# Optimization experiments

Measured on AMD Instinct MI355X. Metric: run time of the kernel, lower is better.

Reference implementation:

```python
import jax, jax.numpy as jnp
import numpy as np

MARGIN = 0.2
EPS = 1e-6  # F.pairwise_distance default eps (added to the difference)


def _cdist(x):
    # Euclidean pairwise distances, [N, N]
    sq = jnp.sum(x * x, axis=1)
    d2 = sq[:, None] + sq[None, :] - 2.0 * (x @ x.T)
    return jnp.sqrt(jnp.maximum(d2, 0.0))


def setup_inputs() -> dict:
    key = jax.random.key(0)
    k1, k2 = jax.random.split(key)
    features = jax.random.normal(k1, (8192, 128), dtype=jnp.float32)
    labels = jax.random.randint(k2, (8192,), 0, 512)
    return {"features": features, "labels": labels}


def reference(features, labels):
    # Distances are used only for (non-differentiable) index selection.
    dists = jax.lax.stop_gradient(_cdist(features))
    pos_mask = labels[None, :] == labels[:, None]  # includes diagonal (self), as in the torch loop
    neg_mask = ~pos_mask

    # Batch-hard mining, vectorized over all anchor rows:
    # hardest positive = max dist among same-label; hardest negative = min dist among different-label.
    pos_idx = jnp.argmax(jnp.where(pos_mask, dists, -jnp.inf), axis=1)
    neg_idx = jnp.argmin(jnp.where(neg_mask, dists, jnp.inf), axis=1)
    # Anchor is skipped in the original loop only if it has no negatives.
    valid = jnp.any(neg_mask, axis=1)

    anchors = features
    pos = features[pos_idx]
    neg = features[neg_idx]

    # F.pairwise_distance(x1, x2, p=2) == ||x1 - x2 + eps||_2
    pos_d = jnp.linalg.norm(anchors - pos + EPS, axis=1)
    neg_d = jnp.linalg.norm(anchors - neg + EPS, axis=1)
    per_anchor = jax.nn.relu(pos_d - neg_d + MARGIN)

    cnt = jnp.sum(valid)
    loss = jnp.where(
        cnt > 0,
        jnp.sum(jnp.where(valid, per_anchor, 0.0)) / jnp.maximum(cnt, 1).astype(per_anchor.dtype),
        jnp.zeros((), per_anchor.dtype),
    )
    return loss
```

## Files before the change

kernel.cpp:

```cpp
#include <hip/hip_runtime.h>
#include <hip/hip_bf16.h>

#define N 8192
#define DIMS 128
#define NSLICE 16
#define SLICE_COLS (N / NSLICE)
#define SUBTILES (SLICE_COLS / 16)
#define NSTEPS (SUBTILES / 2)
#define ROWS_PER_BLOCK 128
#define STRIPS 2
#define NROWBLK (N / ROWS_PER_BLOCK)
#define NFIN 2048
#define MARGIN_F 0.2f
#define EPS_F 1e-6f
#define INF_F __builtin_huge_valf()

typedef __bf16 bf16x8 __attribute__((ext_vector_type(8)));
typedef float f32x4 __attribute__((ext_vector_type(4)));

#define XB_OFF   0
#define META_OFF 2097152
#define PART_OFF 2162688
#define BSUM_OFF 4259840

#define GLD_LDS(g, l) \
  __builtin_amdgcn_global_load_lds( \
      (const __attribute__((address_space(1))) void*)(g), \
      (__attribute__((address_space(3))) void*)(l), 16, 0, 0)

__global__ __launch_bounds__(256) void prep_kernel(
    const float* __restrict__ feat, const int* __restrict__ lab,
    unsigned short* __restrict__ Xb, float2* __restrict__ meta) {
  int row = blockIdx.x * 4 + (threadIdx.x >> 6);
  int lane = threadIdx.x & 63;
  float2 x = *reinterpret_cast<const float2*>(feat + (size_t)row * DIMS + lane * 2);
  __hip_bfloat16 hx = __float2bfloat16(x.x);
  __hip_bfloat16 hy = __float2bfloat16(x.y);
  unsigned short ux, uy;
  __builtin_memcpy(&ux, &hx, 2);
  __builtin_memcpy(&uy, &hy, 2);
  unsigned int packed = (unsigned int)ux | ((unsigned int)uy << 16);
  *reinterpret_cast<unsigned int*>(Xb + (size_t)row * DIMS + lane * 2) = packed;
  float s = x.x * x.x + x.y * x.y;
#pragma unroll
  for (int m = 32; m >= 1; m >>= 1) s += __shfl_xor(s, m, 64);
  if (lane == 0) meta[row] = make_float2(s, __int_as_float(lab[row]));
}

__global__ __launch_bounds__(256, 4) void mine_kernel(
    const unsigned short* __restrict__ Xb, const float2* __restrict__ meta,
    const int* __restrict__ lab, float4* __restrict__ part) {
  __shared__ char smem[2 * 8192 + 4096];

  int rb = blockIdx.x / NSLICE;
  int sl = blockIdx.x % NSLICE;
  int tid = threadIdx.x;
  int wave = tid >> 6;
  int lane = tid & 63;
  int lrow = lane & 15;
  int lk = lane >> 4;
  int rowbase = rb * ROWS_PER_BLOCK + wave * (STRIPS * 16);
  int j0 = sl * SLICE_COLS;

  {
    const char* g = (const char*)meta + (size_t)j0 * 8 + tid * 16;
    char* l = smem + 16384 + wave * 1024;
    GLD_LDS(g, l);
  }
  int colt = tid >> 4;
  int chunk = tid & 15;
  const char* gsrc0 = (const char*)Xb + (size_t)(j0 + colt) * 256 +
                      ((chunk ^ (colt & 7)) * 16);
  {
    GLD_LDS(gsrc0, smem + wave * 1024);
    GLD_LDS(gsrc0 + 16 * 256, smem + 4096 + wave * 1024);
  }

  bf16x8 afrag[STRIPS][4];
#pragma unroll
  for (int s = 0; s < STRIPS; ++s) {
    const unsigned short* rp = Xb + (size_t)(rowbase + s * 16 + lrow) * DIMS;
#pragma unroll
    for (int g = 0; g < 4; ++g)
      afrag[s][g] = *reinterpret_cast<const bf16x8*>(rp + g * 32 + lk * 8);
  }
  int4 labi[STRIPS];
#pragma unroll
  for (int s = 0; s < STRIPS; ++s)
    labi[s] = *reinterpret_cast<const int4*>(lab + rowbase + s * 16 + lk * 4);

  float bpv[STRIPS][4], bnv[STRIPS][4];
  int bpi[STRIPS][4], bni[STRIPS][4];
#pragma unroll
  for (int s = 0; s < STRIPS; ++s)
#pragma unroll
    for (int e = 0; e < 4; ++e) {
      bpv[s][e] = -INF_F; bnv[s][e] = INF_F; bpi[s][e] = 0; bni[s][e] = 0;
    }

  int boff[4];
#pragma unroll
  for (int g = 0; g < 4; ++g)
    boff[g] = lrow * 256 + (((g * 4 + lk) ^ (lrow & 7)) * 16);

  __syncthreads();

  for (int it = 0; it < NSTEPS; ++it) {
    int cur = it & 1;
    if (it + 1 < NSTEPS) {
      const char* g = gsrc0 + (size_t)(it + 1) * 8192;
      char* l = smem + (cur ^ 1) * 8192 + wave * 1024;
      GLD_LDS(g, l);
      GLD_LDS(g + 16 * 256, l + 4096);
    }

#pragma unroll
    for (int h = 0; h < 2; ++h) {
      int t = it * 2 + h;
      float2 mcur =
          *reinterpret_cast<const float2*>(smem + 16384 + t * 128 + lrow * 8);
      float sqj = mcur.x;
      int labj = __float_as_int(mcur.y);
      int jcur = j0 + t * 16 + lrow;

      const char* bbase = smem + cur * 8192 + h * 4096;
      bf16x8 bb[4];
#pragma unroll
      for (int g = 0; g < 4; ++g)
        bb[g] = *reinterpret_cast<const bf16x8*>(bbase + boff[g]);

#pragma unroll
      for (int s = 0; s < STRIPS; ++s) {
        f32x4 acc = {0.f, 0.f, 0.f, 0.f};
#pragma unroll
        for (int g = 0; g < 4; ++g)
          acc = __builtin_amdgcn_mfma_f32_16x16x32_bf16(afrag[s][g], bb[g], acc,
                                                        0, 0, 0);
        int labs[4] = {labi[s].x, labi[s].y, labi[s].z, labi[s].w};
#pragma unroll
        for (int e = 0; e < 4; ++e) {
          float key = fmaf(-2.0f, acc[e], sqj);
          bool pos = (labj == labs[e]);
          bool gp = pos && (key > bpv[s][e]);
          bool gn = (!pos) && (key < bnv[s][e]);
          bpv[s][e] = gp ? key : bpv[s][e];
          bpi[s][e] = gp ? jcur : bpi[s][e];
          bnv[s][e] = gn ? key : bnv[s][e];
          bni[s][e] = gn ? jcur : bni[s][e];
        }
      }
    }
    __syncthreads();
  }

#pragma unroll
  for (int s = 0; s < STRIPS; ++s) {
#pragma unroll
    for (int e = 0; e < 4; ++e) {
      float pv = bpv[s][e]; int pi = bpi[s][e];
      float nv = bnv[s][e]; int ni = bni[s][e];
#pragma unroll
      for (int m = 1; m < 16; m <<= 1) {
        float opv = __shfl_xor(pv, m, 64); int opi = __shfl_xor(pi, m, 64);
        float onv = __shfl_xor(nv, m, 64); int oni = __shfl_xor(ni, m, 64);
        bool tp = (opv > pv) || (opv == pv && opi < pi);
        pv = tp ? opv : pv; pi = tp ? opi : pi;
        bool tn = (onv < nv) || (onv == nv && oni < ni);
        nv = tn ? onv : nv; ni = tn ? oni : ni;
      }
      if (lrow == 0) {
        int row = rowbase + s * 16 + lk * 4 + e;
        part[(size_t)sl * N + row] =
            make_float4(pv, __int_as_float(pi), nv, __int_as_float(ni));
      }
    }
  }
}

__global__ __launch_bounds__(256) void finalize_kernel(
    const float* __restrict__ feat, const float4* __restrict__ part,
    float2* __restrict__ bsum) {
  int wave = threadIdx.x >> 6, lane = threadIdx.x & 63;
  int i = blockIdx.x * 4 + wave;

  float pv = -INF_F, nv = INF_F;
  int pi = 0, ni = 0;
  if (lane < NSLICE) {
    float4 p = part[(size_t)lane * N + i];
    pv = p.x; pi = __float_as_int(p.y);
    nv = p.z; ni = __float_as_int(p.w);
  }
#pragma unroll
  for (int m = 1; m < 16; m <<= 1) {
    float opv = __shfl_xor(pv, m, 64); int opi = __shfl_xor(pi, m, 64);
    float onv = __shfl_xor(nv, m, 64); int oni = __shfl_xor(ni, m, 64);
    bool tp = (opv > pv) || (opv == pv && opi < pi);
    pv = tp ? opv : pv; pi = tp ? opi : pi;
    bool tn = (onv < nv) || (onv == nv && oni < ni);
    nv = tn ? onv : nv; ni = tn ? oni : ni;
  }
  pi = __shfl(pi, 0, 64);
  ni = __shfl(ni, 0, 64);
  float nvb = __shfl(nv, 0, 64);
  bool valid = (nvb < INF_F);

  float2 av = *reinterpret_cast<const float2*>(feat + (size_t)i * DIMS + lane * 2);
  float2 pw = *reinterpret_cast<const float2*>(feat + (size_t)pi * DIMS + lane * 2);
  float2 nw = *reinterpret_cast<const float2*>(feat + (size_t)ni * DIMS + lane * 2);
  float d0 = av.x - pw.x + EPS_F, d1 = av.y - pw.y + EPS_F;
  float sp = fmaf(d0, d0, d1 * d1);
  float e0 = av.x - nw.x + EPS_F, e1 = av.y - nw.y + EPS_F;
  float sn = fmaf(e0, e0, e1 * e1);
#pragma unroll
  for (int m = 32; m >= 1; m >>= 1) {
    sp += __shfl_xor(sp, m, 64);
    sn += __shfl_xor(sn, m, 64);
  }

  __shared__ float s_s[4], s_c[4];
  if (lane == 0) {
    float per = sqrtf(sp) - sqrtf(sn) + MARGIN_F;
    per = per > 0.f ? per : 0.f;
    per = valid ? per : 0.f;
    s_s[wave] = per;
    s_c[wave] = valid ? 1.f : 0.f;
  }
  __syncthreads();
  if (threadIdx.x == 0) {
    float ts = (s_s[0] + s_s[1]) + (s_s[2] + s_s[3]);
    float tc = (s_c[0] + s_c[1]) + (s_c[2] + s_c[3]);
    bsum[blockIdx.x] = make_float2(ts, tc);
  }
}

__global__ __launch_bounds__(256) void final_reduce_kernel(
    const float2* __restrict__ bsum, float* __restrict__ out) {
  int t = threadIdx.x;
  float s = 0.f, c = 0.f;
#pragma unroll
  for (int k = 0; k < NFIN / 256; ++k) {
    float2 v = bsum[t + k * 256];
    s += v.x; c += v.y;
  }
#pragma unroll
  for (int m = 32; m >= 1; m >>= 1) {
    s += __shfl_xor(s, m, 64);
    c += __shfl_xor(c, m, 64);
  }
  __shared__ float s_s[4], s_c[4];
  int wave = t >> 6, lane = t & 63;
  if (lane == 0) { s_s[wave] = s; s_c[wave] = c; }
  __syncthreads();
  if (t == 0) {
    float ts = (s_s[0] + s_s[1]) + (s_s[2] + s_s[3]);
    float tc = (s_c[0] + s_c[1]) + (s_c[2] + s_c[3]);
    out[0] = (tc > 0.f) ? (ts / tc) : 0.f;
  }
}

extern "C" void kernel_launch(void* const* d_in, const int* in_sizes, int n_in,
                              void* d_out, int out_size, void* d_ws, size_t ws_size,
                              hipStream_t stream) {
  const float* feat = (const float*)d_in[0];
  const int* lab = (const int*)d_in[1];
  char* ws = (char*)d_ws;
  unsigned short* Xb = (unsigned short*)(ws + XB_OFF);
  float2* meta = (float2*)(ws + META_OFF);
  float4* part = (float4*)(ws + PART_OFF);
  float2* bsum = (float2*)(ws + BSUM_OFF);
  float* out = (float*)d_out;

  prep_kernel<<<N / 4, 256, 0, stream>>>(feat, lab, Xb, meta);
  mine_kernel<<<NROWBLK * NSLICE, 256, 0, stream>>>(Xb, meta, lab, part);
  finalize_kernel<<<N / 4, 256, 0, stream>>>(feat, part, bsum);
  final_reduce_kernel<<<1, 256, 0, stream>>>(bsum, out);
}
```

Baseline: 49.46 us.

## Pack distance key and column index into one uint for integer max/min mining

Adds a positive bias to the squared norms so that every distance key stays positive. Each key's float bits are truncated and the 13-bit column index is ORed into the low bits, so the argmax/argmin tracking becomes a single unsigned max/min per element. This removes the separate compare/select of value and index, halves the partial-result storage, and simplifies both shuffle reductions. The tiling also changes to 256 rows per block with 4 strips and 32 column slices, which raises register reuse but lowers occupancy. Truncating the low mantissa bits can change ties and near-ties in hard-example selection, and it relies on the bias keeping keys positive for these inputs.

```diff
diff --git a/kernel.cpp b/kernel.cpp
--- a/kernel.cpp
+++ b/kernel.cpp
@@ -3,16 +3,17 @@
 
 #define N 8192
 #define DIMS 128
-#define NSLICE 16
+#define NSLICE 32
 #define SLICE_COLS (N / NSLICE)
 #define SUBTILES (SLICE_COLS / 16)
 #define NSTEPS (SUBTILES / 2)
-#define ROWS_PER_BLOCK 128
-#define STRIPS 2
+#define ROWS_PER_BLOCK 256
+#define STRIPS 4
 #define NROWBLK (N / ROWS_PER_BLOCK)
 #define NFIN 2048
 #define MARGIN_F 0.2f
 #define EPS_F 1e-6f
+#define BIAS_F 512.0f
 #define INF_F __builtin_huge_valf()
 
 typedef __bf16 bf16x8 __attribute__((ext_vector_type(8)));
@@ -44,13 +45,13 @@
   float s = x.x * x.x + x.y * x.y;
 #pragma unroll
   for (int m = 32; m >= 1; m >>= 1) s += __shfl_xor(s, m, 64);
-  if (lane == 0) meta[row] = make_float2(s, __int_as_float(lab[row]));
-}
-
-__global__ __launch_bounds__(256, 4) void mine_kernel(
+  if (lane == 0) meta[row] = make_float2(s + BIAS_F, __int_as_float(lab[row]));
+}
+
+__global__ __launch_bounds__(256, 3) void mine_kernel(
     const unsigned short* __restrict__ Xb, const float2* __restrict__ meta,
-    const int* __restrict__ lab, float4* __restrict__ part) {
-  __shared__ char smem[2 * 8192 + 4096];
+    const int* __restrict__ lab, uint2* __restrict__ part) {
+  __shared__ char smem[2 * 8192 + 2048];
 
   int rb = blockIdx.x / NSLICE;
   int sl = blockIdx.x % NSLICE;
@@ -62,7 +63,7 @@
   int rowbase = rb * ROWS_PER_BLOCK + wave * (STRIPS * 16);
   int j0 = sl * SLICE_COLS;
 
-  {
+  if (wave < 2) {
     const char* g = (const char*)meta + (size_t)j0 * 8 + tid * 16;
     char* l = smem + 16384 + wave * 1024;
     GLD_LDS(g, l);
@@ -73,7 +74,7 @@
                       ((chunk ^ (colt & 7)) * 16);
   {
     GLD_LDS(gsrc0, smem + wave * 1024);
-    GLD_LDS(gsrc0 + 16 * 256, smem + 4096 + wave * 1024);
+    GLD_LDS(gsrc0 + 4096, smem + 4096 + wave * 1024);
   }
 
   bf16x8 afrag[STRIPS][4];
@@ -89,14 +90,11 @@
   for (int s = 0; s < STRIPS; ++s)
     labi[s] = *reinterpret_cast<const int4*>(lab + rowbase + s * 16 + lk * 4);
 
-  float bpv[STRIPS][4], bnv[STRIPS][4];
-  int bpi[STRIPS][4], bni[STRIPS][4];
+  unsigned int bpu[STRIPS][4], bnu[STRIPS][4];
 #pragma unroll
   for (int s = 0; s < STRIPS; ++s)
 #pragma unroll
-    for (int e = 0; e < 4; ++e) {
-      bpv[s][e] = -INF_F; bnv[s][e] = INF_F; bpi[s][e] = 0; bni[s][e] = 0;
-    }
+    for (int e = 0; e < 4; ++e) { bpu[s][e] = 0u; bnu[s][e] = 0xFFFFFFFFu; }
 
   int boff[4];
 #pragma unroll
@@ -111,7 +109,7 @@
       const char* g = gsrc0 + (size_t)(it + 1) * 8192;
       char* l = smem + (cur ^ 1) * 8192 + wave * 1024;
       GLD_LDS(g, l);
-      GLD_LDS(g + 16 * 256, l + 4096);
+      GLD_LDS(g + 4096, l + 4096);
     }
 
 #pragma unroll
@@ -119,9 +117,9 @@
       int t = it * 2 + h;
       float2 mcur =
           *reinterpret_cast<const float2*>(smem + 16384 + t * 128 + lrow * 8);
-      float sqj = mcur.x;
+      float sqjB = mcur.x;
       int labj = __float_as_int(mcur.y);
-      int jcur = j0 + t * 16 + lrow;
+      unsigned int ju = (unsigned int)(j0 + t * 16 + lrow);
 
       const char* bbase = smem + cur * 8192 + h * 4096;
       bf16x8 bb[4];
@@ -139,14 +137,13 @@
         int labs[4] = {labi[s].x, labi[s].y, labi[s].z, labi[s].w};
 #pragma unroll
         for (int e = 0; e < 4; ++e) {
-          float key = fmaf(-2.0f, acc[e], sqj);
+          float key = fmaf(-2.0f, acc[e], sqjB);
+          unsigned int u = (__float_as_uint(key) & 0xFFFFE000u) | ju;
           bool pos = (labj == labs[e]);
-          bool gp = pos && (key > bpv[s][e]);
-          bool gn = (!pos) && (key < bnv[s][e]);
-          bpv[s][e] = gp ? key : bpv[s][e];
-          bpi[s][e] = gp ? jcur : bpi[s][e];
-          bnv[s][e] = gn ? key : bnv[s][e];
-          bni[s][e] = gn ? jcur : bni[s][e];
+          unsigned int up = pos ? u : 0u;
+          unsigned int un = pos ? 0xFFFFFFFFu : u;
+          bpu[s][e] = max(bpu[s][e], up);
+          bnu[s][e] = min(bnu[s][e], un);
         }
       }
     }
@@ -157,52 +154,41 @@
   for (int s = 0; s < STRIPS; ++s) {
 #pragma unroll
     for (int e = 0; e < 4; ++e) {
-      float pv = bpv[s][e]; int pi = bpi[s][e];
-      float nv = bnv[s][e]; int ni = bni[s][e];
+      unsigned int pu = bpu[s][e], nu = bnu[s][e];
 #pragma unroll
       for (int m = 1; m < 16; m <<= 1) {
-        float opv = __shfl_xor(pv, m, 64); int opi = __shfl_xor(pi, m, 64);
-        float onv = __shfl_xor(nv, m, 64); int oni = __shfl_xor(ni, m, 64);
-        bool tp = (opv > pv) || (opv == pv && opi < pi);
-        pv = tp ? opv : pv; pi = tp ? opi : pi;
-        bool tn = (onv < nv) || (onv == nv && oni < ni);
-        nv = tn ? onv : nv; ni = tn ? oni : ni;
+        pu = max(pu, (unsigned int)__shfl_xor((int)pu, m, 64));
+        nu = min(nu, (unsigned int)__shfl_xor((int)nu, m, 64));
       }
       if (lrow == 0) {
         int row = rowbase + s * 16 + lk * 4 + e;
-        part[(size_t)sl * N + row] =
-            make_float4(pv, __int_as_float(pi), nv, __int_as_float(ni));
+        part[(size_t)sl * N + row] = make_uint2(pu, nu);
       }
     }
   }
 }
 
 __global__ __launch_bounds__(256) void finalize_kernel(
-    const float* __restrict__ feat, const float4* __restrict__ part,
+    const float* __restrict__ feat, const uint2* __restrict__ part,
     float2* __restrict__ bsum) {
   int wave = threadIdx.x >> 6, lane = threadIdx.x & 63;
   int i = blockIdx.x * 4 + wave;
 
-  float pv = -INF_F, nv = INF_F;
-  int pi = 0, ni = 0;
+  unsigned int pu = 0u, nu = 0xFFFFFFFFu;
   if (lane < NSLICE) {
-    float4 p = part[(size_t)lane * N + i];
-    pv = p.x; pi = __float_as_int(p.y);
-    nv = p.z; ni = __float_as_int(p.w);
-  }
-#pragma unroll
-  for (int m = 1; m < 16; m <<= 1) {
-    float opv = __shfl_xor(pv, m, 64); int opi = __shfl_xor(pi, m, 64);
-    float onv = __shfl_xor(nv, m, 64); int oni = __shfl_xor(ni, m, 64);
-    bool tp = (opv > pv) || (opv == pv && opi < pi);
-    pv = tp ? opv : pv; pi = tp ? opi : pi;
-    bool tn = (onv < nv) || (onv == nv && oni < ni);
-    nv = tn ? onv : nv; ni = tn ? oni : ni;
-  }
-  pi = __shfl(pi, 0, 64);
-  ni = __shfl(ni, 0, 64);
-  float nvb = __shfl(nv, 0, 64);
-  bool valid = (nvb < INF_F);
+    uint2 p = part[(size_t)lane * N + i];
+    pu = p.x; nu = p.y;
+  }
+#pragma unroll
+  for (int m = 1; m < 32; m <<= 1) {
+    pu = max(pu, (unsigned int)__shfl_xor((int)pu, m, 64));
+    nu = min(nu, (unsigned int)__shfl_xor((int)nu, m, 64));
+  }
+  pu = (unsigned int)__shfl((int)pu, 0, 64);
+  nu = (unsigned int)__shfl((int)nu, 0, 64);
+  bool valid = (nu != 0xFFFFFFFFu);
+  int pi = (int)(pu & 8191u);
+  int ni = (int)(nu & 8191u);
 
   float2 av = *reinterpret_cast<const float2*>(feat + (size_t)i * DIMS + lane * 2);
   float2 pw = *reinterpret_cast<const float2*>(feat + (size_t)pi * DIMS + lane * 2);
@@ -266,7 +252,7 @@
   char* ws = (char*)d_ws;
   unsigned short* Xb = (unsigned short*)(ws + XB_OFF);
   float2* meta = (float2*)(ws + META_OFF);
-  float4* part = (float4*)(ws + PART_OFF);
+  uint2* part = (uint2*)(ws + PART_OFF);
   float2* bsum = (float2*)(ws + BSUM_OFF);
   float* out = (float*)d_out;
 
```

After: 47.71 us. 3.5% less time.
